# Optimization experiments

Hardware: AMD Instinct MI355X
Metric: run time of the kernel (lower is better)

The kernel has to match this reference:

```python
import jax, jax.numpy as jnp
import numpy as np

VOCAB = 256  # vocab_size from init_kwargs
B, W, L = 256, 512, 20  # batch sentences, words per sentence, chars per word


def setup_inputs() -> dict:
    key = jax.random.key(0)
    k1, k2 = jax.random.split(key)
    char_ids = jax.random.randint(k1, (B, W, L), 0, VOCAB, dtype=jnp.int32)
    # nn.Parameter scalar forgetting factor (learned); nonzero init avoids 0^0 grad nan
    forgetting_factor = jax.random.uniform(k2, (1,), dtype=jnp.float32)
    return {"char_ids": char_ids, "forgetting_factor": forgetting_factor}


def reference(char_ids, forgetting_factor):
    # z_k = alpha * z_{k-1} + onehot(char_k)  unrolls to
    # z_L = sum_k alpha^(L-1-k) * onehot(char_k)
    b, w, l = char_ids.shape
    alpha = forgetting_factor[0]
    powers = alpha ** jnp.arange(l - 1, -1, -1, dtype=jnp.float32)  # [L]
    flat_ids = char_ids.reshape(b * w, l)  # [BW, L]
    rows = jnp.arange(b * w, dtype=jnp.int32)[:, None]  # [BW, 1]
    out = jnp.zeros((b * w, VOCAB), dtype=powers.dtype)
    out = out.at[rows, flat_ids].add(jnp.broadcast_to(powers, (b * w, l)))
    return out.reshape(b, w, VOCAB)
```

## Files before the change

### kernel.cpp

```cpp
#include <hip/hip_runtime.h>


constexpr int L = 20;
constexpr int VOCAB = 256;
constexpr int BLOCK = 256;
constexpr int GRID = 2048;

__global__ __launch_bounds__(BLOCK) void fofe_kernel(
    const int* __restrict__ char_ids,
    const float* __restrict__ alpha_ptr,
    float* __restrict__ out,
    int n_rows)
{
    __shared__ float sm[(BLOCK / 64) * VOCAB];

    const int lane            = threadIdx.x & 63;
    const int wave            = threadIdx.x >> 6;
    const int waves_per_block = BLOCK >> 6;
    const int wave_id         = blockIdx.x * waves_per_block + wave;
    const int total_waves     = gridDim.x * waves_per_block;

    const float alpha = *alpha_ptr;

    float pw = 1.0f;
    {
        float cur = 1.0f;
        #pragma unroll
        for (int e = 0; e < L; ++e) {
            if (lane == (L - 1) - e) pw = cur;
            cur *= alpha;
        }
    }

    float*  smw = sm + wave * VOCAB;
    float4* sm4 = (float4*)smw;
    float4* out4 = (float4*)out;

    const int iters = (n_rows + total_waves - 1) / total_waves;
    for (int it = 0; it < iters; ++it) {
        const int  row    = wave_id + it * total_waves;
        const bool active = row < n_rows;

        if (active) sm4[lane] = make_float4(0.f, 0.f, 0.f, 0.f);
        __syncthreads();

        if (active && lane < L) {
            const int id = char_ids[(size_t)row * L + lane];
            atomicAdd(&smw[id], pw);
        }
        __syncthreads();

        if (active) {
            out4[(size_t)row * (VOCAB / 4) + lane] = sm4[lane];
        }
        __syncthreads();
    }
}

extern "C" void kernel_launch(void* const* d_in, const int* in_sizes, int n_in,
                              void* d_out, int out_size, void* d_ws, size_t ws_size,
                              hipStream_t stream) {
    const int*   char_ids = (const int*)d_in[0];
    const float* alpha    = (const float*)d_in[1];
    float*       out      = (float*)d_out;
    const int    n_rows   = in_sizes[0] / L;

    fofe_kernel<<<GRID, BLOCK, 0, stream>>>(char_ids, alpha, out, n_rows);
}
```

Baseline: 149.8 us.

## Process two rows per wave, prefetch next ids, drop block barriers

Each wave now handles a pair of rows per iteration, using 40 of 64 lanes for the scatter and writing 512 floats per pass. The char ids for the next pair are loaded early so global-load latency overlaps the current pair's work. All __syncthreads are replaced by compiler memory barriers, relying on wave-level lockstep within each wave's private shared slice. This removes block-wide synchronisation and halves loop overhead, but assumes n_rows is even and that wave-synchronous LDS ordering holds without explicit waits.

After: 147.0 us. No clear change (-1.9%).

```diff
diff --git a/kernel.cpp b/kernel.cpp
--- a/kernel.cpp
+++ b/kernel.cpp
@@ -1,10 +1,11 @@
 #include <hip/hip_runtime.h>
 
 
-constexpr int L = 20;
+constexpr int L     = 20;
 constexpr int VOCAB = 256;
 constexpr int BLOCK = 256;
-constexpr int GRID = 2048;
+constexpr int GRID  = 2048;
+constexpr int R     = 2;
 
 __global__ __launch_bounds__(BLOCK) void fofe_kernel(
     const int* __restrict__ char_ids,
@@ -12,48 +13,63 @@
     float* __restrict__ out,
     int n_rows)
 {
-    __shared__ float sm[(BLOCK / 64) * VOCAB];
+    __shared__ float sm[(BLOCK / 64) * R * VOCAB];
 
-    const int lane            = threadIdx.x & 63;
-    const int wave            = threadIdx.x >> 6;
-    const int waves_per_block = BLOCK >> 6;
-    const int wave_id         = blockIdx.x * waves_per_block + wave;
-    const int total_waves     = gridDim.x * waves_per_block;
+    const int lane        = threadIdx.x & 63;
+    const int wave        = threadIdx.x >> 6;
+    const int wave_id     = blockIdx.x * (BLOCK >> 6) + wave;
+    const int total_waves = gridDim.x * (BLOCK >> 6);
 
     const float alpha = *alpha_ptr;
+
+    const int sub = (lane >= L) ? 1 : 0;
+    const int ch  = lane - sub * L;
 
     float pw = 1.0f;
     {
         float cur = 1.0f;
         #pragma unroll
         for (int e = 0; e < L; ++e) {
-            if (lane == (L - 1) - e) pw = cur;
+            if (ch == (L - 1) - e) pw = cur;
             cur *= alpha;
         }
     }
 
-    float*  smw = sm + wave * VOCAB;
-    float4* sm4 = (float4*)smw;
+    float*  smw  = sm + wave * (R * VOCAB);
+    float4* sm4  = (float4*)smw;
     float4* out4 = (float4*)out;
 
-    const int iters = (n_rows + total_waves - 1) / total_waves;
-    for (int it = 0; it < iters; ++it) {
-        const int  row    = wave_id + it * total_waves;
-        const bool active = row < n_rows;
+    const int n_pairs = n_rows / R;
+    const bool scat   = lane < R * L;
 
-        if (active) sm4[lane] = make_float4(0.f, 0.f, 0.f, 0.f);
-        __syncthreads();
+    int id_cur = 0;
+    if (wave_id < n_pairs && scat)
+        id_cur = char_ids[(size_t)wave_id * (R * L) + lane];
 
-        if (active && lane < L) {
-            const int id = char_ids[(size_t)row * L + lane];
-            atomicAdd(&smw[id], pw);
-        }
-        __syncthreads();
+    for (int pair = wave_id; pair < n_pairs; pair += total_waves) {
+        sm4[lane]      = make_float4(0.f, 0.f, 0.f, 0.f);
+        sm4[lane + 64] = make_float4(0.f, 0.f, 0.f, 0.f);
 
-        if (active) {
-            out4[(size_t)row * (VOCAB / 4) + lane] = sm4[lane];
-        }
-        __syncthreads();
+        const int next_pair = pair + total_waves;
+        int id_next = 0;
+        if (next_pair < n_pairs && scat)
+            id_next = char_ids[(size_t)next_pair * (R * L) + lane];
+
+        asm volatile("" ::: "memory");
+
+        if (scat)
+            atomicAdd(&smw[sub * VOCAB + id_cur], pw);
+
+        asm volatile("" ::: "memory");
+
+        const float4 v0 = sm4[lane];
+        const float4 v1 = sm4[lane + 64];
+        const size_t o  = (size_t)pair * (R * VOCAB / 4);
+        out4[o + lane]      = v0;
+        out4[o + 64 + lane] = v1;
+
+        id_cur = id_next;
+        asm volatile("" ::: "memory");
     }
 }
 
```
